# Kernel optimization log

Hardware: AMD Instinct MI355X
Metric: run time of the kernel (lower is better)

## Reference

```python
import jax, jax.numpy as jnp
import numpy as np
import math

T, B, E, H = 1024, 4, 512, 8
HD = E // H

def setup_inputs() -> dict:
    key = jax.random.key(0)
    ks = jax.random.split(key, 6)
    return {
        "query": jax.random.normal(ks[0], (T, B, E), dtype=jnp.float32),
        "dist": jax.random.normal(ks[1], (B, T, T, H), dtype=jnp.float32) * 0.1,
        "in_proj_weight": jax.random.normal(ks[2], (3 * E, E), dtype=jnp.float32) * 0.02,
        "in_proj_bias": jax.random.normal(ks[3], (3 * E,), dtype=jnp.float32) * 0.02,
        "out_proj_weight": jax.random.normal(ks[4], (E, E), dtype=jnp.float32) * 0.02,
        "out_proj_bias": jax.random.normal(ks[5], (E,), dtype=jnp.float32) * 0.02,
    }

def reference(query, dist, in_proj_weight, in_proj_bias, out_proj_weight, out_proj_bias):
    t, b, e = query.shape
    # packed in-projection (self-attention: q=k=v=query)
    qkv = query @ in_proj_weight.T + in_proj_bias          # [T,B,3E]
    q, k, v = jnp.split(qkv, 3, axis=-1)                   # each [T,B,E]
    def heads(x):
        return x.reshape(t, b * H, HD).transpose(1, 0, 2)  # [B*H,T,HD]
    q, k, v = heads(q), heads(k), heads(v)
    q = q / math.sqrt(HD)
    attn = jnp.einsum('bte,bse->bts', q, k)                # [B*H,T,T]
    # distance/structure bias: [B,T,T,H] -> [B,H,T,T] -> [B*H,T,T]
    bias = jnp.transpose(dist, (0, 3, 1, 2)).reshape(b * H, t, t)
    attn = jax.nn.softmax(attn + bias, axis=-1)
    out = jnp.einsum('bts,bse->bte', attn, v)              # [B*H,T,HD]
    out = out.transpose(1, 0, 2).reshape(t, b, e)          # [T,B,E]
    out = out @ out_proj_weight.T + out_proj_bias
    return out
```

## Files before the change

### kernel.cpp

```cpp
#include <hip/hip_runtime.h>
#include <math.h>

typedef __bf16 bf16;
typedef bf16 bf16x8 __attribute__((ext_vector_type(8)));
typedef bf16 bf16x4 __attribute__((ext_vector_type(4)));
typedef float f32x4 __attribute__((ext_vector_type(4)));

#define T_DIM 1024
#define B_DIM 4
#define E_DIM 512
#define H_DIM 8
#define HD_DIM 64
#define BH_DIM 32

__device__ __forceinline__ f32x4 mfma16(bf16x8 a, bf16x8 b, f32x4 c) {
    return __builtin_amdgcn_mfma_f32_16x16x32_bf16(a, b, c, 0, 0, 0);
}

__device__ __forceinline__ bf16x4 cvt4(f32x4 v) {
    bf16x4 o;
    o[0] = (bf16)v[0]; o[1] = (bf16)v[1]; o[2] = (bf16)v[2]; o[3] = (bf16)v[3];
    return o;
}

#define CVT_Q_V   524288
#define CVT_W1_V  196608
__global__ __launch_bounds__(256)
void cvt_all(const float* __restrict__ q, const float* __restrict__ w1,
             const float* __restrict__ w2, bf16* __restrict__ qo,
             bf16* __restrict__ w1o, bf16* __restrict__ w2o) {
    long v = (long)blockIdx.x * 256 + threadIdx.x;
    const float* src; bf16* dst;
    if (v < CVT_Q_V)                { src = q;  dst = qo; }
    else if (v < CVT_Q_V + CVT_W1_V){ v -= CVT_Q_V;  src = w1; dst = w1o; }
    else                            { v -= CVT_Q_V + CVT_W1_V; src = w2; dst = w2o; }
    f32x4 f = *(const f32x4*)(src + v * 4);
    *(bf16x4*)(dst + v * 4) = cvt4(f);
}

__global__ __launch_bounds__(256)
void bias_transpose(const float* __restrict__ dist, bf16* __restrict__ bias_t) {
    __shared__ __align__(16) bf16 tile[8 * 1032];
    const int bt = blockIdx.x;
    const int b = bt >> 10, t = bt & 1023;
    const int tid = threadIdx.x;
    const float* src = dist + ((long)bt << 13) + tid * 32;
    const int s0 = tid * 4;
    float v[32];
#pragma unroll
    for (int j = 0; j < 8; j++) {
        f32x4 f = *(const f32x4*)(src + j * 4);
        v[j * 4 + 0] = f[0]; v[j * 4 + 1] = f[1];
        v[j * 4 + 2] = f[2]; v[j * 4 + 3] = f[3];
    }
#pragma unroll
    for (int h = 0; h < 8; h++)
#pragma unroll
        for (int si = 0; si < 4; si++)
            tile[h * 1032 + s0 + si] = (bf16)v[si * 8 + h];
    __syncthreads();
#pragma unroll
    for (int rep = 0; rep < 4; rep++) {
        int slot = rep * 256 + tid;
        int h = slot >> 7;
        int sc = (slot & 127) * 8;
        bf16x8 o = *(const bf16x8*)&tile[h * 1032 + sc];
        *(bf16x8*)&bias_t[((long)(b * 8 + h) * T_DIM + t) * T_DIM + sc] = o;
    }
}

template<int TM, int TN, int MODE>
__global__ __launch_bounds__(256)
void gemm_t(const bf16* __restrict__ A, const bf16* __restrict__ Bt,
            const float* __restrict__ bias, int K, int N,
            float* __restrict__ out, bf16* __restrict__ qb,
            bf16* __restrict__ kb, bf16* __restrict__ vb) {
    constexpr int FM = TM / 32, FN = TN / 32;
    __shared__ __align__(16) bf16 As[TM * 72];
    __shared__ __align__(16) bf16 Bs[TN * 72];
    const int tid  = threadIdx.x;
    const int lane = tid & 63;
    const int wave = tid >> 6;
    const int quad = lane >> 4;
    const int l15  = lane & 15;
    const int wm = wave & 1, wn = wave >> 1;
    const int m0 = blockIdx.x * TM, n0 = blockIdx.y * TN;

    f32x4 acc[FM][FN] = {};

    const int sr = tid >> 2;
    const int sc = (tid & 3) * 16;

    for (int k0 = 0; k0 < K; k0 += 64) {
#pragma unroll
        for (int p = 0; p < TM / 64; p++) {
            const bf16* src = &A[(long)(m0 + p * 64 + sr) * K + k0 + sc];
            *(bf16x8*)&As[(p * 64 + sr) * 72 + sc]     = *(const bf16x8*)(src);
            *(bf16x8*)&As[(p * 64 + sr) * 72 + sc + 8] = *(const bf16x8*)(src + 8);
        }
#pragma unroll
        for (int p = 0; p < TN / 64; p++) {
            const bf16* src = &Bt[(long)(n0 + p * 64 + sr) * K + k0 + sc];
            *(bf16x8*)&Bs[(p * 64 + sr) * 72 + sc]     = *(const bf16x8*)(src);
            *(bf16x8*)&Bs[(p * 64 + sr) * 72 + sc + 8] = *(const bf16x8*)(src + 8);
        }
        __syncthreads();
#pragma unroll
        for (int kk = 0; kk < 64; kk += 32) {
            bf16x8 af[FM], bf[FN];
#pragma unroll
            for (int mb = 0; mb < FM; mb++)
                af[mb] = *(const bf16x8*)&As[(wm * (TM / 2) + mb * 16 + l15) * 72 + kk + quad * 8];
#pragma unroll
            for (int nb = 0; nb < FN; nb++)
                bf[nb] = *(const bf16x8*)&Bs[(wn * (TN / 2) + nb * 16 + l15) * 72 + kk + quad * 8];
#pragma unroll
            for (int mb = 0; mb < FM; mb++)
#pragma unroll
                for (int nb = 0; nb < FN; nb++)
                    acc[mb][nb] = mfma16(af[mb], bf[nb], acc[mb][nb]);
        }
        __syncthreads();
    }

#pragma unroll
    for (int mb = 0; mb < FM; mb++) {
#pragma unroll
        for (int nb = 0; nb < FN; nb++) {
            int n = n0 + wn * (TN / 2) + nb * 16 + l15;
            float bv = bias[n];
#pragma unroll
            for (int r = 0; r < 4; r++) {
                int m = m0 + wm * (TM / 2) + mb * 16 + quad * 4 + r;
                float v = acc[mb][nb][r] + bv;
                if (MODE == 0) {
                    out[(long)m * N + n] = v;
                } else {
                    int t = m >> 2, b = m & 3;
                    int sec = n >> 9, j = n & 511;
                    int h = j >> 6, hd = j & 63;
                    int bh = b * 8 + h;
                    if (sec == 0)
                        qb[((long)bh * T_DIM + t) * HD_DIM + hd] = (bf16)(v * 0.125f);
                    else if (sec == 1)
                        kb[((long)bh * T_DIM + t) * HD_DIM + hd] = (bf16)v;
                    else
                        vb[((long)bh * HD_DIM + hd) * T_DIM + t] = (bf16)v;
                }
            }
        }
    }
}

__global__ __launch_bounds__(256)
void attn_kernel(const bf16* __restrict__ qb, const bf16* __restrict__ kb,
                 const bf16* __restrict__ vb, const bf16* __restrict__ bias_t,
                 float* __restrict__ ctx) {
    __shared__ __align__(16) bf16 Ks[64 * 72];
    __shared__ __align__(16) bf16 Vts[64 * 72];
    __shared__ __align__(16) bf16 Bs[64 * 72];
    __shared__ __align__(16) bf16 Ps[4 * 16 * 72];
    const int tid  = threadIdx.x;
    const int lane = tid & 63;
    const int wave = tid >> 6;
    const int quad = lane >> 4;
    const int l15  = lane & 15;
    const int bid = blockIdx.x;
    const int bh  = bid >> 4;
    const int qt  = bid & 15;
    const int b   = bh >> 3, h = bh & 7;
    const int qrow = qt * 64 + wave * 16 + l15;

    bf16x8 qa0 = *(const bf16x8*)&qb[((long)bh * T_DIM + qrow) * HD_DIM + quad * 8];
    bf16x8 qa1 = *(const bf16x8*)&qb[((long)bh * T_DIM + qrow) * HD_DIM + 32 + quad * 8];

    f32x4 oacc[4] = {};
    float lsum[4] = {0.f, 0.f, 0.f, 0.f};

    const int r0 = tid >> 3;
    const int c0 = (tid & 7) * 8;

    const bf16* biasrow0 = &bias_t[((long)bh * T_DIM + qt * 64 + r0) * T_DIM];
    const bf16* biasrow1 = &bias_t[((long)bh * T_DIM + qt * 64 + r0 + 32) * T_DIM];

    bf16x8 pk0, pk1, pv0, pv1, pb0, pb1;
    pk0 = *(const bf16x8*)&kb[((long)bh * T_DIM + r0) * HD_DIM + c0];
    pk1 = *(const bf16x8*)&kb[((long)bh * T_DIM + r0 + 32) * HD_DIM + c0];
    pv0 = *(const bf16x8*)&vb[((long)bh * HD_DIM + r0) * T_DIM + c0];
    pv1 = *(const bf16x8*)&vb[((long)bh * HD_DIM + r0 + 32) * T_DIM + c0];
    pb0 = *(const bf16x8*)&biasrow0[c0];
    pb1 = *(const bf16x8*)&biasrow1[c0];

    for (int st = 0; st < T_DIM; st += 64) {
        __syncthreads();
        *(bf16x8*)&Ks[r0 * 72 + c0]         = pk0;
        *(bf16x8*)&Ks[(r0 + 32) * 72 + c0]  = pk1;
        *(bf16x8*)&Vts[r0 * 72 + c0]        = pv0;
        *(bf16x8*)&Vts[(r0 + 32) * 72 + c0] = pv1;
        *(bf16x8*)&Bs[r0 * 72 + c0]         = pb0;
        *(bf16x8*)&Bs[(r0 + 32) * 72 + c0]  = pb1;
        __syncthreads();

        if (st + 64 < T_DIM) {
            const int sn = st + 64;
            pk0 = *(const bf16x8*)&kb[((long)bh * T_DIM + sn + r0) * HD_DIM + c0];
            pk1 = *(const bf16x8*)&kb[((long)bh * T_DIM + sn + r0 + 32) * HD_DIM + c0];
            pv0 = *(const bf16x8*)&vb[((long)bh * HD_DIM + r0) * T_DIM + sn + c0];
            pv1 = *(const bf16x8*)&vb[((long)bh * HD_DIM + r0 + 32) * T_DIM + sn + c0];
            pb0 = *(const bf16x8*)&biasrow0[sn + c0];
            pb1 = *(const bf16x8*)&biasrow1[sn + c0];
        }

        f32x4 sacc[4] = {};
#pragma unroll
        for (int kk = 0; kk < 64; kk += 32) {
            bf16x8 a = (kk == 0) ? qa0 : qa1;
#pragma unroll
            for (int nb = 0; nb < 4; nb++) {
                bf16x8 bfr = *(const bf16x8*)&Ks[(nb * 16 + l15) * 72 + kk + quad * 8];
                sacc[nb] = mfma16(a, bfr, sacc[nb]);
            }
        }

        bf16* pw = &Ps[wave * 16 * 72];
#pragma unroll
        for (int r = 0; r < 4; r++) {
            const int tl = wave * 16 + quad * 4 + r;
            float rs = 0.f;
#pragma unroll
            for (int nb = 0; nb < 4; nb++) {
                float d = (float)Bs[tl * 72 + nb * 16 + l15];
                float p = __expf(sacc[nb][r] + d);
                rs += p;
                pw[(quad * 4 + r) * 72 + nb * 16 + l15] = (bf16)p;
            }
            lsum[r] += rs;
        }

#pragma unroll
        for (int kk = 0; kk < 64; kk += 32) {
            bf16x8 ap = *(const bf16x8*)&pw[l15 * 72 + kk + quad * 8];
#pragma unroll
            for (int nb = 0; nb < 4; nb++) {
                bf16x8 bv2 = *(const bf16x8*)&Vts[(nb * 16 + l15) * 72 + kk + quad * 8];
                oacc[nb] = mfma16(ap, bv2, oacc[nb]);
            }
        }
    }

#pragma unroll
    for (int r = 0; r < 4; r++) {
#pragma unroll
        for (int msk = 1; msk < 16; msk <<= 1)
            lsum[r] += __shfl_xor(lsum[r], msk);
    }

#pragma unroll
    for (int nb = 0; nb < 4; nb++) {
#pragma unroll
        for (int r = 0; r < 4; r++) {
            int t  = qt * 64 + wave * 16 + quad * 4 + r;
            int hd = nb * 16 + l15;
            float o = oacc[nb][r] / lsum[r];
            ctx[((long)t * B_DIM + b) * E_DIM + h * HD_DIM + hd] = o;
        }
    }
}

__global__ __launch_bounds__(256)
void cvt_ctx(const float* __restrict__ src, bf16* __restrict__ dst) {
    long v = (long)blockIdx.x * 256 + threadIdx.x;
    f32x4 f = *(const f32x4*)(src + v * 4);
    *(bf16x4*)(dst + v * 4) = cvt4(f);
}

extern "C" void kernel_launch(void* const* d_in, const int* in_sizes, int n_in,
                              void* d_out, int out_size, void* d_ws, size_t ws_size,
                              hipStream_t stream) {
    const float* query = (const float*)d_in[0];
    const float* dist  = (const float*)d_in[1];
    const float* win   = (const float*)d_in[2];
    const float* bin   = (const float*)d_in[3];
    const float* wout  = (const float*)d_in[4];
    const float* bout  = (const float*)d_in[5];
    float* out = (float*)d_out;

    bf16* bias_t = (bf16*)d_ws;
    bf16* qb   = bias_t + ((long)BH_DIM * T_DIM * T_DIM);
    bf16* kb   = qb + (1 << 21);
    bf16* vb   = kb + (1 << 21);
    float* ctx = (float*)(vb + (1 << 21));
    bf16* qbf  = (bf16*)(ctx + (1 << 21));
    bf16* w1bf = qbf + (1 << 21);
    bf16* w2bf = w1bf + 786432;
    bf16* ctxb = w2bf + 262144;

    cvt_all<<<dim3(3072), 256, 0, stream>>>(query, win, wout, qbf, w1bf, w2bf);
    bias_transpose<<<dim3(B_DIM * T_DIM), 256, 0, stream>>>(dist, bias_t);
    gemm_t<128, 128, 1><<<dim3(32, 12), 256, 0, stream>>>(
        qbf, w1bf, bin, 512, 1536, nullptr, qb, kb, vb);
    attn_kernel<<<dim3(512), 256, 0, stream>>>(qb, kb, vb, bias_t, ctx);
    cvt_ctx<<<dim3(2048), 256, 0, stream>>>(ctx, ctxb);
    gemm_t<128, 64, 0><<<dim3(32, 8), 256, 0, stream>>>(
        ctxb, w2bf, bout, 512, 512, out, nullptr, nullptr, nullptr);
}
```

Baseline: 288.3 us.

## Fuse dist bias read and ctx bf16 conversion into attention kernel

Drops the separate bias_transpose kernel: the attention kernel now reads fp32 dist directly from its [B,T,T,H] layout into registers, prefetched one tile ahead. The ctx conversion kernel is also removed by writing bf16 context straight from attention, and s_setprio hints are added around the MFMA blocks. This avoids writing and re-reading a 64 MB bf16 bias tensor and one extra launch. The cost is strided 4-byte gathers with a stride of 8 floats, which use only part of each fetched cache line, and more registers per thread.

```diff
diff --git a/kernel.cpp b/kernel.cpp
--- a/kernel.cpp
+++ b/kernel.cpp
@@ -36,37 +36,6 @@
     else                            { v -= CVT_Q_V + CVT_W1_V; src = w2; dst = w2o; }
     f32x4 f = *(const f32x4*)(src + v * 4);
     *(bf16x4*)(dst + v * 4) = cvt4(f);
-}
-
-__global__ __launch_bounds__(256)
-void bias_transpose(const float* __restrict__ dist, bf16* __restrict__ bias_t) {
-    __shared__ __align__(16) bf16 tile[8 * 1032];
-    const int bt = blockIdx.x;
-    const int b = bt >> 10, t = bt & 1023;
-    const int tid = threadIdx.x;
-    const float* src = dist + ((long)bt << 13) + tid * 32;
-    const int s0 = tid * 4;
-    float v[32];
-#pragma unroll
-    for (int j = 0; j < 8; j++) {
-        f32x4 f = *(const f32x4*)(src + j * 4);
-        v[j * 4 + 0] = f[0]; v[j * 4 + 1] = f[1];
-        v[j * 4 + 2] = f[2]; v[j * 4 + 3] = f[3];
-    }
-#pragma unroll
-    for (int h = 0; h < 8; h++)
-#pragma unroll
-        for (int si = 0; si < 4; si++)
-            tile[h * 1032 + s0 + si] = (bf16)v[si * 8 + h];
-    __syncthreads();
-#pragma unroll
-    for (int rep = 0; rep < 4; rep++) {
-        int slot = rep * 256 + tid;
-        int h = slot >> 7;
-        int sc = (slot & 127) * 8;
-        bf16x8 o = *(const bf16x8*)&tile[h * 1032 + sc];
-        *(bf16x8*)&bias_t[((long)(b * 8 + h) * T_DIM + t) * T_DIM + sc] = o;
-    }
 }
 
 template<int TM, int TN, int MODE>
@@ -154,11 +123,10 @@
 
 __global__ __launch_bounds__(256)
 void attn_kernel(const bf16* __restrict__ qb, const bf16* __restrict__ kb,
-                 const bf16* __restrict__ vb, const bf16* __restrict__ bias_t,
-                 float* __restrict__ ctx) {
+                 const bf16* __restrict__ vb, const float* __restrict__ dist,
+                 bf16* __restrict__ ctxb) {
     __shared__ __align__(16) bf16 Ks[64 * 72];
     __shared__ __align__(16) bf16 Vts[64 * 72];
-    __shared__ __align__(16) bf16 Bs[64 * 72];
     __shared__ __align__(16) bf16 Ps[4 * 16 * 72];
     const int tid  = threadIdx.x;
     const int lane = tid & 63;
@@ -180,16 +148,19 @@
     const int r0 = tid >> 3;
     const int c0 = (tid & 7) * 8;
 
-    const bf16* biasrow0 = &bias_t[((long)bh * T_DIM + qt * 64 + r0) * T_DIM];
-    const bf16* biasrow1 = &bias_t[((long)bh * T_DIM + qt * 64 + r0 + 32) * T_DIM];
-
-    bf16x8 pk0, pk1, pv0, pv1, pb0, pb1;
+    const float* dp = dist + (long)(b * 1024 + qt * 64 + wave * 16 + quad * 4) * 8192 + h;
+
+    bf16x8 pk0, pk1, pv0, pv1;
+    float pbias[16];
     pk0 = *(const bf16x8*)&kb[((long)bh * T_DIM + r0) * HD_DIM + c0];
     pk1 = *(const bf16x8*)&kb[((long)bh * T_DIM + r0 + 32) * HD_DIM + c0];
     pv0 = *(const bf16x8*)&vb[((long)bh * HD_DIM + r0) * T_DIM + c0];
     pv1 = *(const bf16x8*)&vb[((long)bh * HD_DIM + r0 + 32) * T_DIM + c0];
-    pb0 = *(const bf16x8*)&biasrow0[c0];
-    pb1 = *(const bf16x8*)&biasrow1[c0];
+#pragma unroll
+    for (int r = 0; r < 4; r++)
+#pragma unroll
+        for (int nb = 0; nb < 4; nb++)
+            pbias[r * 4 + nb] = dp[(long)r * 8192 + (nb * 16 + l15) * 8];
 
     for (int st = 0; st < T_DIM; st += 64) {
         __syncthreads();
@@ -197,8 +168,6 @@
         *(bf16x8*)&Ks[(r0 + 32) * 72 + c0]  = pk1;
         *(bf16x8*)&Vts[r0 * 72 + c0]        = pv0;
         *(bf16x8*)&Vts[(r0 + 32) * 72 + c0] = pv1;
-        *(bf16x8*)&Bs[r0 * 72 + c0]         = pb0;
-        *(bf16x8*)&Bs[(r0 + 32) * 72 + c0]  = pb1;
         __syncthreads();
 
         if (st + 64 < T_DIM) {
@@ -207,11 +176,10 @@
             pk1 = *(const bf16x8*)&kb[((long)bh * T_DIM + sn + r0 + 32) * HD_DIM + c0];
             pv0 = *(const bf16x8*)&vb[((long)bh * HD_DIM + r0) * T_DIM + sn + c0];
             pv1 = *(const bf16x8*)&vb[((long)bh * HD_DIM + r0 + 32) * T_DIM + sn + c0];
-            pb0 = *(const bf16x8*)&biasrow0[sn + c0];
-            pb1 = *(const bf16x8*)&biasrow1[sn + c0];
         }
 
         f32x4 sacc[4] = {};
+        __builtin_amdgcn_s_setprio(1);
 #pragma unroll
         for (int kk = 0; kk < 64; kk += 32) {
             bf16x8 a = (kk == 0) ? qa0 : qa1;
@@ -221,22 +189,31 @@
                 sacc[nb] = mfma16(a, bfr, sacc[nb]);
             }
         }
+        __builtin_amdgcn_s_setprio(0);
 
         bf16* pw = &Ps[wave * 16 * 72];
 #pragma unroll
         for (int r = 0; r < 4; r++) {
-            const int tl = wave * 16 + quad * 4 + r;
             float rs = 0.f;
 #pragma unroll
             for (int nb = 0; nb < 4; nb++) {
-                float d = (float)Bs[tl * 72 + nb * 16 + l15];
-                float p = __expf(sacc[nb][r] + d);
+                float p = __expf(sacc[nb][r] + pbias[r * 4 + nb]);
                 rs += p;
                 pw[(quad * 4 + r) * 72 + nb * 16 + l15] = (bf16)p;
             }
             lsum[r] += rs;
         }
 
+        if (st + 64 < T_DIM) {
+            const int sn = st + 64;
+#pragma unroll
+            for (int r = 0; r < 4; r++)
+#pragma unroll
+                for (int nb = 0; nb < 4; nb++)
+                    pbias[r * 4 + nb] = dp[(long)r * 8192 + (sn + nb * 16 + l15) * 8];
+        }
+
+        __builtin_amdgcn_s_setprio(1);
 #pragma unroll
         for (int kk = 0; kk < 64; kk += 32) {
             bf16x8 ap = *(const bf16x8*)&pw[l15 * 72 + kk + quad * 8];
@@ -246,6 +223,7 @@
                 oacc[nb] = mfma16(ap, bv2, oacc[nb]);
             }
         }
+        __builtin_amdgcn_s_setprio(0);
     }
 
 #pragma unroll
@@ -262,16 +240,9 @@
             int t  = qt * 64 + wave * 16 + quad * 4 + r;
             int hd = nb * 16 + l15;
             float o = oacc[nb][r] / lsum[r];
-            ctx[((long)t * B_DIM + b) * E_DIM + h * HD_DIM + hd] = o;
-        }
-    }
-}
-
-__global__ __launch_bounds__(256)
-void cvt_ctx(const float* __restrict__ src, bf16* __restrict__ dst) {
-    long v = (long)blockIdx.x * 256 + threadIdx.x;
-    f32x4 f = *(const f32x4*)(src + v * 4);
-    *(bf16x4*)(dst + v * 4) = cvt4(f);
+            ctxb[((long)t * B_DIM + b) * E_DIM + h * HD_DIM + hd] = (bf16)o;
+        }
+    }
 }
 
 extern "C" void kernel_launch(void* const* d_in, const int* in_sizes, int n_in,
@@ -285,22 +256,18 @@
     const float* bout  = (const float*)d_in[5];
     float* out = (float*)d_out;
 
-    bf16* bias_t = (bf16*)d_ws;
-    bf16* qb   = bias_t + ((long)BH_DIM * T_DIM * T_DIM);
+    bf16* qb   = (bf16*)d_ws;
     bf16* kb   = qb + (1 << 21);
     bf16* vb   = kb + (1 << 21);
-    float* ctx = (float*)(vb + (1 << 21));
-    bf16* qbf  = (bf16*)(ctx + (1 << 21));
+    bf16* qbf  = vb + (1 << 21);
     bf16* w1bf = qbf + (1 << 21);
     bf16* w2bf = w1bf + 786432;
     bf16* ctxb = w2bf + 262144;
 
     cvt_all<<<dim3(3072), 256, 0, stream>>>(query, win, wout, qbf, w1bf, w2bf);
-    bias_transpose<<<dim3(B_DIM * T_DIM), 256, 0, stream>>>(dist, bias_t);
     gemm_t<128, 128, 1><<<dim3(32, 12), 256, 0, stream>>>(
         qbf, w1bf, bin, 512, 1536, nullptr, qb, kb, vb);
-    attn_kernel<<<dim3(512), 256, 0, stream>>>(qb, kb, vb, bias_t, ctx);
-    cvt_ctx<<<dim3(2048), 256, 0, stream>>>(ctx, ctxb);
+    attn_kernel<<<dim3(512), 256, 0, stream>>>(qb, kb, vb, dist, ctxb);
     gemm_t<128, 64, 0><<<dim3(32, 8), 256, 0, stream>>>(
         ctxb, w2bf, bout, 512, 512, out, nullptr, nullptr, nullptr);
 }
```

Result: faster. 280.6 us (-2.7%).
